# Performance work log

Measured on AMD Instinct MI355X. Metric: run time of the kernel, lower is better.

Reference implementation:

```python
import jax, jax.numpy as jnp
import numpy as np


def quat_to_rot(q):
    # q: [B, 4] = (x, y, z, w); same math as from_quaternion in the source.
    x, y, z, w = q[:, 0], q[:, 1], q[:, 2], q[:, 3]
    tx, ty, tz = 2.0 * x, 2.0 * y, 2.0 * z
    twx, twy, twz = tx * w, ty * w, tz * w
    txx, txy, txz = tx * x, ty * x, tz * x
    tyy, tyz, tzz = ty * y, tz * y, tz * z
    r = jnp.stack([1.0 - (tyy + tzz), txy - twz, txz + twy,
                   txy + twz, 1.0 - (txx + tzz), tyz - twx,
                   txz - twy, tyz + twx, 1.0 - (txx + tyy)], axis=-1)
    return r.reshape(-1, 3, 3)


def matrix_from_params(transfos):
    B, N = transfos.shape
    R = quat_to_rot(transfos[:, :4])
    if N == 10:
        S = jax.vmap(jnp.diag)(transfos[:, -3:])
    else:
        S = jnp.broadcast_to(jnp.eye(3, dtype=transfos.dtype), (B, 3, 3))
    SR = jnp.matmul(S, R)
    if N == 7:
        t = transfos[:, 4:7][..., None]
    else:
        t = jnp.zeros((B, 3, 1), transfos.dtype)
    return jnp.concatenate([SR, t], axis=2)  # [B, 3, 4]


def spatial_transformer_3d(img, transfos, min_ref_grid, max_ref_grid):
    B, H, W, D, C = img.shape  # ref_size_xyz = (W, H, D) per the source
    theta = matrix_from_params(transfos)  # [B, 3, 4]

    xs = jnp.linspace(min_ref_grid[0], max_ref_grid[0], W)
    ys = jnp.linspace(min_ref_grid[1], max_ref_grid[1], H)
    zs = jnp.linspace(min_ref_grid[2], max_ref_grid[2], D)
    mz, my, mx = jnp.meshgrid(zs, ys, xs, indexing='ij')  # (D, H, W), x fastest
    Nel = D * H * W
    grid = jnp.stack([mx.ravel(), my.ravel(), mz.ravel(),
                      jnp.ones(Nel, dtype=img.dtype)], axis=0)  # (4, Nel)
    pts = jnp.einsum('bij,jn->bin', theta, grid)  # (B, 3, Nel)

    Wf, Hf, Df = float(W), float(H), float(D)
    cx = (Wf - 1.0) / (max_ref_grid[0] - min_ref_grid[0])
    cy = (Hf - 1.0) / (max_ref_grid[1] - min_ref_grid[1])
    cz = (Df - 1.0) / (max_ref_grid[2] - min_ref_grid[2])
    ix = cx * pts[:, 0, :] - cx * min_ref_grid[0]
    iy = cy * pts[:, 1, :] - cy * min_ref_grid[1]
    iz = cz * pts[:, 2, :] - cz * min_ref_grid[2]

    # padding_mode in {'zeros','min'}: validity mask for out-of-grid points
    valid = ((ix >= 0.0) & (ix <= Wf - 1.0) &
             (iy >= 0.0) & (iy <= Hf - 1.0) &
             (iz >= 0.0) & (iz <= Df - 1.0)).astype(img.dtype)[..., None]  # (B, Nel, 1)

    ix0 = jnp.clip(jnp.floor(ix), 0.0, Wf - 1.0)
    iy0 = jnp.clip(jnp.floor(iy), 0.0, Hf - 1.0)
    iz0 = jnp.clip(jnp.floor(iz), 0.0, Df - 1.0)

    imf = img.reshape(B, H * W * D, C)
    acc = jnp.zeros((B, Nel, C), img.dtype)
    for ox in (0.0, 1.0):
        for oy in (0.0, 1.0):
            for oz in (0.0, 1.0):
                gx, gy, gz = ix0 + ox, iy0 + oy, iz0 + oz  # corner coords
                w = (jnp.clip(1.0 - jnp.abs(ix - gx), 0.0, 1.0) *
                     jnp.clip(1.0 - jnp.abs(iy - gy), 0.0, 1.0) *
                     jnp.clip(1.0 - jnp.abs(iz - gz), 0.0, 1.0))
                gxi = jnp.clip(gx, 0.0, Wf - 1.0).astype(jnp.int32)
                gyi = jnp.clip(gy, 0.0, Hf - 1.0).astype(jnp.int32)
                gzi = jnp.clip(gz, 0.0, Df - 1.0).astype(jnp.int32)
                lin = (gyi * W + gxi) * D + gzi  # row-major index into [H, W, D]
                v = jnp.take_along_axis(imf, lin[..., None], axis=1)  # (B, Nel, C)
                acc = acc + w[..., None] * v

    # padding_mode == 'min': fill out-of-grid voxels with the per-volume minimum
    fill = jnp.min(img, axis=(1, 2, 3, 4))[:, None, None]  # (B, 1, 1)
    out = valid * acc + (1.0 - valid) * fill
    # grid was flattened in (z, y, x) order with x fastest -> back to (H, W, D)
    out = out.reshape(B, D, H, W, C).transpose(0, 2, 3, 1, 4)
    return out


def setup_inputs() -> dict:
    key = jax.random.key(0)
    k1, k2 = jax.random.split(key)
    img = jax.random.normal(k1, (4, 160, 160, 160, 1), dtype=jnp.float32)
    transfos = jax.random.normal(k2, (4, 7), dtype=jnp.float32)
    return {"img": img, "transfos": transfos}


def reference(img, transfos):
    min_ref_grid = (-1.0, -1.0, -1.0)
    max_ref_grid = (1.0, 1.0, 1.0)
    return spatial_transformer_3d(img, transfos, min_ref_grid, max_ref_grid)
```

## Files before the change

### kernel.cpp

```cpp
#include <hip/hip_runtime.h>

#define HH 160
#define WW 160
#define DD 160
#define BB 4
#define NPB (HH * WW * DD / 4)
#define K1B 256

typedef float vfloat4 __attribute__((ext_vector_type(4)));

__global__ __launch_bounds__(256) void min_cst_kernel(const float4* __restrict__ img4,
                                                      const float* __restrict__ transfos,
                                                      float* __restrict__ partial,
                                                      double* __restrict__ cst) {
    const int b = blockIdx.y;
    const size_t base = (size_t)b * NPB;
    const int t0 = blockIdx.x * 256 + threadIdx.x;
    const int S = K1B * 256;

    float m = 3.4e38f;
    #pragma unroll
    for (int r = 0; r < 4; r++) {
        const int i0 = t0 + 4 * r * S;
        float4 v0 = img4[base + i0];
        float4 v1 = img4[base + i0 + S];
        float4 v2 = img4[base + i0 + 2 * S];
        float4 v3 = make_float4(3.4e38f, 3.4e38f, 3.4e38f, 3.4e38f);
        if (i0 + 3 * S < NPB) v3 = img4[base + i0 + 3 * S];
        m = fminf(m, fminf(fminf(v0.x, v0.y), fminf(v0.z, v0.w)));
        m = fminf(m, fminf(fminf(v1.x, v1.y), fminf(v1.z, v1.w)));
        m = fminf(m, fminf(fminf(v2.x, v2.y), fminf(v2.z, v2.w)));
        m = fminf(m, fminf(fminf(v3.x, v3.y), fminf(v3.z, v3.w)));
    }

    #pragma unroll
    for (int o = 32; o >= 1; o >>= 1) m = fminf(m, __shfl_down(m, o));
    __shared__ float s[4];
    const int lane = threadIdx.x & 63, wid = threadIdx.x >> 6;
    if (lane == 0) s[wid] = m;
    __syncthreads();
    if (threadIdx.x == 0) {
        partial[b * K1B + blockIdx.x] =
            fminf(fminf(s[0], s[1]), fminf(s[2], s[3]));
    }

    if (blockIdx.x == 0 && blockIdx.y == 0 && threadIdx.x < BB) {
        const int bb = threadIdx.x;
        const float* q = transfos + bb * 7;
        double x = q[0], y = q[1], z = q[2], w = q[3];
        double tx = 2.0 * x, ty = 2.0 * y, tz = 2.0 * z;
        double twx = tx * w, twy = ty * w, twz = tz * w;
        double txx = tx * x, txy = ty * x, txz = tz * x;
        double tyy = ty * y, tyz = tz * y, tzz = tz * z;
        double R[3][3] = {
            {1.0 - (tyy + tzz), txy - twz,         txz + twy},
            {txy + twz,         1.0 - (txx + tzz), tyz - twx},
            {txz - twy,         tyz + twx,         1.0 - (txx + tyy)}
        };
        double t[3] = {(double)q[4], (double)q[5], (double)q[6]};
        for (int r = 0; r < 3; r++) {
            cst[bb * 12 + r * 4 + 0] = R[r][0];
            cst[bb * 12 + r * 4 + 1] = R[r][1];
            cst[bb * 12 + r * 4 + 2] = R[r][2];
            cst[bb * 12 + r * 4 + 3] = 79.5 * (t[r] - R[r][0] - R[r][1] - R[r][2] + 1.0);
        }
    }
}

__global__ __launch_bounds__(256) void fin_min_kernel(const float* __restrict__ partial,
                                                      float* __restrict__ fill) {
    const int wid = threadIdx.x >> 6, lane = threadIdx.x & 63;
    const float* p = partial + wid * K1B;
    float m = fminf(fminf(p[lane], p[lane + 64]), fminf(p[lane + 128], p[lane + 192]));
    #pragma unroll
    for (int o = 32; o >= 1; o >>= 1) m = fminf(m, __shfl_down(m, o));
    if (lane == 0) fill[wid] = m;
}

__global__ __launch_bounds__(256) void fill_kernel(const float* __restrict__ fill,
                                                   float* __restrict__ out) {
    const int b = blockIdx.y;
    const float fv = fill[b];
    vfloat4 v; v[0] = fv; v[1] = fv; v[2] = fv; v[3] = fv;
    vfloat4* o = (vfloat4*)(out + (size_t)b * (HH * WW * DD));
    const int stride = gridDim.x * 256;
    for (int i = blockIdx.x * 256 + threadIdx.x; i < NPB; i += stride)
        __builtin_nontemporal_store(v, o + i);
}

__global__ __launch_bounds__(256) void st3d_kernel(const float* __restrict__ img,
                                                   const double* __restrict__ cst,
                                                   const float* __restrict__ fill,
                                                   float* __restrict__ out) {
    const int bzc = blockIdx.z;
    const int b = bzc / 20;
    const int yt = bzc - b * 20;

    const double* c = cst + b * 12;
    const double c2 = c[2], c6 = c[6], c10 = c[10];

    {
        const double X0 = (double)(blockIdx.y * 8), X1 = X0 + 7.0;
        const double Y0 = (double)(yt * 8),         Y1 = Y0 + 7.0;
        const double Z0 = (double)(blockIdx.x * 16), Z1 = Z0 + 15.0;
        double lo, hi, t;

        lo = c[3]; hi = c[3];
        t = c[0]; if (t >= 0.0) { lo += t * X0; hi += t * X1; } else { lo += t * X1; hi += t * X0; }
        t = c[1]; if (t >= 0.0) { lo += t * Y0; hi += t * Y1; } else { lo += t * Y1; hi += t * Y0; }
        t = c2;   if (t >= 0.0) { lo += t * Z0; hi += t * Z1; } else { lo += t * Z1; hi += t * Z0; }
        if (hi < -1e-3 || lo > 159.001) return;

        lo = c[7]; hi = c[7];
        t = c[4]; if (t >= 0.0) { lo += t * X0; hi += t * X1; } else { lo += t * X1; hi += t * X0; }
        t = c[5]; if (t >= 0.0) { lo += t * Y0; hi += t * Y1; } else { lo += t * Y1; hi += t * Y0; }
        t = c6;   if (t >= 0.0) { lo += t * Z0; hi += t * Z1; } else { lo += t * Z1; hi += t * Z0; }
        if (hi < -1e-3 || lo > 159.001) return;

        lo = c[11]; hi = c[11];
        t = c[8]; if (t >= 0.0) { lo += t * X0; hi += t * X1; } else { lo += t * X1; hi += t * X0; }
        t = c[9]; if (t >= 0.0) { lo += t * Y0; hi += t * Y1; } else { lo += t * Y1; hi += t * Y0; }
        t = c10;  if (t >= 0.0) { lo += t * Z0; hi += t * Z1; } else { lo += t * Z1; hi += t * Z0; }
        if (hi < -1e-3 || lo > 159.001) return;
    }

    const int tz = threadIdx.x & 3;
    const int tx = (threadIdx.x >> 2) & 7;
    const int ty = threadIdx.x >> 5;

    const int x  = blockIdx.y * 8 + tx;
    const int y  = yt * 8 + ty;
    const int zq = blockIdx.x * 16 + tz * 4;

    const float fillv = fill[b];

    const double dx = (double)x, dy = (double)y, dz = (double)zq;
    double ixd = fma(c[0], dx, fma(c[1], dy, fma(c2, dz, c[3])));
    double iyd = fma(c[4], dx, fma(c[5], dy, fma(c6, dz, c[7])));
    double izd = fma(c[8], dx, fma(c[9], dy, fma(c10, dz, c[11])));

    bool anyv = false;
    {
        double ax = ixd, ay = iyd, az = izd;
        #pragma unroll
        for (int k = 0; k < 4; k++) {
            anyv = anyv || ((ax >= 0.0) && (ax <= 159.0) && (ay >= 0.0) &&
                            (ay <= 159.0) && (az >= 0.0) && (az <= 159.0));
            ax += c2; ay += c6; az += c10;
        }
    }

    const float* base = img + (size_t)b * (HH * WW * DD);
    vfloat4 r;

    if (__any(anyv)) {
        #pragma unroll
        for (int k = 0; k < 4; k++) {
            const bool valid = (ixd >= 0.0) && (ixd <= 159.0) && (iyd >= 0.0) &&
                               (iyd <= 159.0) && (izd >= 0.0) && (izd <= 159.0);
            double flx = floor(ixd), fly = floor(iyd), flz = floor(izd);
            int x0 = (int)flx, y0 = (int)fly, z0 = (int)flz;
            x0 = min(max(x0, 0), 159);
            y0 = min(max(y0, 0), 159);
            z0 = min(max(z0, 0), 159);
            float fx = (float)(ixd - flx), fy = (float)(iyd - fly), fz = (float)(izd - flz);
            int x1 = min(x0 + 1, 159), y1 = min(y0 + 1, 159), z1 = min(z0 + 1, 159);
            const int o00 = (y0 * WW + x0) * DD;
            const int o01 = (y0 * WW + x1) * DD;
            const int o10 = (y1 * WW + x0) * DD;
            const int o11 = (y1 * WW + x1) * DD;
            float v000 = base[o00 + z0], v001 = base[o00 + z1];
            float v010 = base[o10 + z0], v011 = base[o10 + z1];
            float v100 = base[o01 + z0], v101 = base[o01 + z1];
            float v110 = base[o11 + z0], v111 = base[o11 + z1];
            float wx0 = 1.0f - fx, wx1 = fx;
            float wy0 = 1.0f - fy, wy1 = fy;
            float wz0 = 1.0f - fz, wz1 = fz;
            float acc;
            acc  = ((wx0 * wy0) * wz0) * v000;
            acc += ((wx0 * wy0) * wz1) * v001;
            acc += ((wx0 * wy1) * wz0) * v010;
            acc += ((wx0 * wy1) * wz1) * v011;
            acc += ((wx1 * wy0) * wz0) * v100;
            acc += ((wx1 * wy0) * wz1) * v101;
            acc += ((wx1 * wy1) * wz0) * v110;
            acc += ((wx1 * wy1) * wz1) * v111;
            r[k] = valid ? acc : fillv;
            ixd += c2; iyd += c6; izd += c10;
        }
    } else {
        r[0] = fillv; r[1] = fillv; r[2] = fillv; r[3] = fillv;
    }

    vfloat4* outp = (vfloat4*)(out + (size_t)((b * HH + y) * WW + x) * DD + zq);
    __builtin_nontemporal_store(r, outp);
}

extern "C" void kernel_launch(void* const* d_in, const int* in_sizes, int n_in,
                              void* d_out, int out_size, void* d_ws, size_t ws_size,
                              hipStream_t stream) {
    const float* img = (const float*)d_in[0];
    const float* transfos = (const float*)d_in[1];
    float* out = (float*)d_out;
    float* partial = (float*)d_ws;
    double* cst = (double*)((char*)d_ws + 4096);
    float* fill = (float*)((char*)d_ws + 8192);

    min_cst_kernel<<<dim3(K1B, BB), 256, 0, stream>>>((const float4*)img, transfos,
                                                      partial, cst);
    fin_min_kernel<<<dim3(1), 256, 0, stream>>>(partial, fill);
    fill_kernel<<<dim3(512, BB), 256, 0, stream>>>(fill, out);
    st3d_kernel<<<dim3(DD / 16, WW / 8, (HH / 8) * BB), 256, 0, stream>>>(img, cst,
                                                                          fill, out);
}
```

Measured before the change: 144.3 us.

## Classify tiles, fill only invalid ones, gather over compacted job list

A classification kernel tests each tile against the transformed volume bounds. Tiles that cannot be valid get the fill value written directly. Candidate tiles are appended to a compacted job list through an atomic counter, and a persistent gather kernel processes that list with one wave per two-row slab. This removes the separate full-volume fill pass that the valid tiles later overwrite, and it avoids launching mostly-idle blocks for the gather. In exchange it adds an atomic, an extra workspace requirement, and job-decode overhead, and it falls back to the old path when the workspace is too small.

After: 135.3 us. -6.2%, faster.

```diff
diff --git a/kernel.cpp b/kernel.cpp
--- a/kernel.cpp
+++ b/kernel.cpp
@@ -6,6 +6,12 @@
 #define BB 4
 #define NPB (HH * WW * DD / 4)
 #define K1B 256
+#define NTZ 10
+#define NTX 20
+#define NTY 20
+#define NTILES (BB * NTY * NTX * NTZ)
+#define JCAP (NTILES * 4)
+#define GBLK 2048
 
 typedef float vfloat4 __attribute__((ext_vector_type(4)));
 
@@ -68,13 +74,167 @@
 }
 
 __global__ __launch_bounds__(256) void fin_min_kernel(const float* __restrict__ partial,
-                                                      float* __restrict__ fill) {
+                                                      float* __restrict__ fill,
+                                                      int* __restrict__ counter) {
+    if (threadIdx.x == 0) *counter = 0;
     const int wid = threadIdx.x >> 6, lane = threadIdx.x & 63;
     const float* p = partial + wid * K1B;
     float m = fminf(fminf(p[lane], p[lane + 64]), fminf(p[lane + 128], p[lane + 192]));
     #pragma unroll
     for (int o = 32; o >= 1; o >>= 1) m = fminf(m, __shfl_down(m, o));
     if (lane == 0) fill[wid] = m;
+}
+
+__device__ __forceinline__ bool tile_may_be_valid(const double* c, int xt, int yt, int zt) {
+    const double X0 = (double)(xt * 8), X1 = X0 + 7.0;
+    const double Y0 = (double)(yt * 8), Y1 = Y0 + 7.0;
+    const double Z0 = (double)(zt * 16), Z1 = Z0 + 15.0;
+    double lo, hi, t;
+
+    lo = c[3]; hi = c[3];
+    t = c[0]; if (t >= 0.0) { lo += t * X0; hi += t * X1; } else { lo += t * X1; hi += t * X0; }
+    t = c[1]; if (t >= 0.0) { lo += t * Y0; hi += t * Y1; } else { lo += t * Y1; hi += t * Y0; }
+    t = c[2]; if (t >= 0.0) { lo += t * Z0; hi += t * Z1; } else { lo += t * Z1; hi += t * Z0; }
+    if (hi < -1e-3 || lo > 159.001) return false;
+
+    lo = c[7]; hi = c[7];
+    t = c[4]; if (t >= 0.0) { lo += t * X0; hi += t * X1; } else { lo += t * X1; hi += t * X0; }
+    t = c[5]; if (t >= 0.0) { lo += t * Y0; hi += t * Y1; } else { lo += t * Y1; hi += t * Y0; }
+    t = c[6]; if (t >= 0.0) { lo += t * Z0; hi += t * Z1; } else { lo += t * Z1; hi += t * Z0; }
+    if (hi < -1e-3 || lo > 159.001) return false;
+
+    lo = c[11]; hi = c[11];
+    t = c[8]; if (t >= 0.0) { lo += t * X0; hi += t * X1; } else { lo += t * X1; hi += t * X0; }
+    t = c[9]; if (t >= 0.0) { lo += t * Y0; hi += t * Y1; } else { lo += t * Y1; hi += t * Y0; }
+    t = c[10]; if (t >= 0.0) { lo += t * Z0; hi += t * Z1; } else { lo += t * Z1; hi += t * Z0; }
+    if (hi < -1e-3 || lo > 159.001) return false;
+    return true;
+}
+
+__global__ __launch_bounds__(256) void fill_cls_kernel(const double* __restrict__ cst,
+                                                       const float* __restrict__ fill,
+                                                       float* __restrict__ out,
+                                                       int* __restrict__ counter,
+                                                       int* __restrict__ list) {
+    const int bzc = blockIdx.z;
+    const int b = bzc / NTY;
+    const int yt = bzc - b * NTY;
+    const double* c = cst + b * 12;
+
+    if (tile_may_be_valid(c, blockIdx.y, yt, blockIdx.x)) {
+        if (threadIdx.x == 0) {
+            const int t = ((b * NTY + yt) * NTX + blockIdx.y) * NTZ + blockIdx.x;
+            const int idx = atomicAdd(counter, 4);
+            list[idx + 0] = t * 4 + 0;
+            list[idx + 1] = t * 4 + 1;
+            list[idx + 2] = t * 4 + 2;
+            list[idx + 3] = t * 4 + 3;
+        }
+        return;
+    }
+
+    const float fv = fill[b];
+    vfloat4 v; v[0] = fv; v[1] = fv; v[2] = fv; v[3] = fv;
+    const int tz = threadIdx.x & 3;
+    const int tx = (threadIdx.x >> 2) & 7;
+    const int ty = threadIdx.x >> 5;
+    const int x = blockIdx.y * 8 + tx;
+    const int y = yt * 8 + ty;
+    const int zq = blockIdx.x * 16 + tz * 4;
+    __builtin_nontemporal_store(v, (vfloat4*)(out + (size_t)((b * HH + y) * WW + x) * DD + zq));
+}
+
+__global__ __launch_bounds__(256) void gather_kernel(const float* __restrict__ img,
+                                                     const double* __restrict__ cst,
+                                                     const float* __restrict__ fill,
+                                                     float* __restrict__ out,
+                                                     const int* __restrict__ counter,
+                                                     const int* __restrict__ list) {
+    const int cnt = *counter;
+    const int wid = threadIdx.x >> 6;
+    const int lane = threadIdx.x & 63;
+    const int tz = lane & 3;
+    const int tx = (lane >> 2) & 7;
+    const int tyl = lane >> 5;
+    const int nslots = gridDim.x * 4;
+
+    for (int j = blockIdx.x * 4 + wid; j < cnt; j += nslots) {
+        const int job = list[j];
+        const int t = job >> 2, pair = job & 3;
+        int zt = t % NTZ;
+        int r0i = t / NTZ;
+        int xt = r0i % NTX; r0i /= NTX;
+        int yt = r0i % NTY;
+        const int b = r0i / NTY;
+
+        const int x = xt * 8 + tx;
+        const int y = yt * 8 + pair * 2 + tyl;
+        const int zq = zt * 16 + tz * 4;
+
+        const double* c = cst + b * 12;
+        const double c2 = c[2], c6 = c[6], c10 = c[10];
+        const float fillv = fill[b];
+
+        const double dx = (double)x, dy = (double)y, dz = (double)zq;
+        double ixd = fma(c[0], dx, fma(c[1], dy, fma(c2, dz, c[3])));
+        double iyd = fma(c[4], dx, fma(c[5], dy, fma(c6, dz, c[7])));
+        double izd = fma(c[8], dx, fma(c[9], dy, fma(c10, dz, c[11])));
+
+        bool anyv = false;
+        {
+            double ax = ixd, ay = iyd, az = izd;
+            #pragma unroll
+            for (int k = 0; k < 4; k++) {
+                anyv = anyv || ((ax >= 0.0) && (ax <= 159.0) && (ay >= 0.0) &&
+                                (ay <= 159.0) && (az >= 0.0) && (az <= 159.0));
+                ax += c2; ay += c6; az += c10;
+            }
+        }
+
+        const float* base = img + (size_t)b * (HH * WW * DD);
+        vfloat4 r;
+
+        if (__any(anyv)) {
+            #pragma unroll
+            for (int k = 0; k < 4; k++) {
+                const bool valid = (ixd >= 0.0) && (ixd <= 159.0) && (iyd >= 0.0) &&
+                                   (iyd <= 159.0) && (izd >= 0.0) && (izd <= 159.0);
+                double flx = floor(ixd), fly = floor(iyd), flz = floor(izd);
+                int x0 = (int)flx, y0 = (int)fly, z0 = (int)flz;
+                x0 = min(max(x0, 0), 159);
+                y0 = min(max(y0, 0), 159);
+                z0 = min(max(z0, 0), 159);
+                float fx = (float)(ixd - flx), fy = (float)(iyd - fly), fz = (float)(izd - flz);
+                int x1 = min(x0 + 1, 159), y1 = min(y0 + 1, 159), z1 = min(z0 + 1, 159);
+                const int o00 = (y0 * WW + x0) * DD;
+                const int o01 = (y0 * WW + x1) * DD;
+                const int o10 = (y1 * WW + x0) * DD;
+                const int o11 = (y1 * WW + x1) * DD;
+                float v000 = base[o00 + z0], v001 = base[o00 + z1];
+                float v010 = base[o10 + z0], v011 = base[o10 + z1];
+                float v100 = base[o01 + z0], v101 = base[o01 + z1];
+                float v110 = base[o11 + z0], v111 = base[o11 + z1];
+                float wx0 = 1.0f - fx, wx1 = fx;
+                float wy0 = 1.0f - fy, wy1 = fy;
+                float wz0 = 1.0f - fz, wz1 = fz;
+                float acc;
+                acc  = ((wx0 * wy0) * wz0) * v000;
+                acc += ((wx0 * wy0) * wz1) * v001;
+                acc += ((wx0 * wy1) * wz0) * v010;
+                acc += ((wx0 * wy1) * wz1) * v011;
+                acc += ((wx1 * wy0) * wz0) * v100;
+                acc += ((wx1 * wy0) * wz1) * v101;
+                acc += ((wx1 * wy1) * wz0) * v110;
+                acc += ((wx1 * wy1) * wz1) * v111;
+                r[k] = valid ? acc : fillv;
+                ixd += c2; iyd += c6; izd += c10;
+            }
+        } else {
+            r[0] = fillv; r[1] = fillv; r[2] = fillv; r[3] = fillv;
+        }
+
+        __builtin_nontemporal_store(r, (vfloat4*)(out + (size_t)((b * HH + y) * WW + x) * DD + zq));
+    }
 }
 
 __global__ __launch_bounds__(256) void fill_kernel(const float* __restrict__ fill,
@@ -88,50 +248,23 @@
         __builtin_nontemporal_store(v, o + i);
 }
 
-__global__ __launch_bounds__(256) void st3d_kernel(const float* __restrict__ img,
-                                                   const double* __restrict__ cst,
-                                                   const float* __restrict__ fill,
-                                                   float* __restrict__ out) {
+__global__ __launch_bounds__(256) void st3d_tile_kernel(const float* __restrict__ img,
+                                                        const double* __restrict__ cst,
+                                                        const float* __restrict__ fill,
+                                                        float* __restrict__ out) {
     const int bzc = blockIdx.z;
-    const int b = bzc / 20;
-    const int yt = bzc - b * 20;
-
+    const int b = bzc / NTY;
+    const int yt = bzc - b * NTY;
     const double* c = cst + b * 12;
+    if (!tile_may_be_valid(c, blockIdx.y, yt, blockIdx.x)) return;
+
     const double c2 = c[2], c6 = c[6], c10 = c[10];
-
-    {
-        const double X0 = (double)(blockIdx.y * 8), X1 = X0 + 7.0;
-        const double Y0 = (double)(yt * 8),         Y1 = Y0 + 7.0;
-        const double Z0 = (double)(blockIdx.x * 16), Z1 = Z0 + 15.0;
-        double lo, hi, t;
-
-        lo = c[3]; hi = c[3];
-        t = c[0]; if (t >= 0.0) { lo += t * X0; hi += t * X1; } else { lo += t * X1; hi += t * X0; }
-        t = c[1]; if (t >= 0.0) { lo += t * Y0; hi += t * Y1; } else { lo += t * Y1; hi += t * Y0; }
-        t = c2;   if (t >= 0.0) { lo += t * Z0; hi += t * Z1; } else { lo += t * Z1; hi += t * Z0; }
-        if (hi < -1e-3 || lo > 159.001) return;
-
-        lo = c[7]; hi = c[7];
-        t = c[4]; if (t >= 0.0) { lo += t * X0; hi += t * X1; } else { lo += t * X1; hi += t * X0; }
-        t = c[5]; if (t >= 0.0) { lo += t * Y0; hi += t * Y1; } else { lo += t * Y1; hi += t * Y0; }
-        t = c6;   if (t >= 0.0) { lo += t * Z0; hi += t * Z1; } else { lo += t * Z1; hi += t * Z0; }
-        if (hi < -1e-3 || lo > 159.001) return;
-
-        lo = c[11]; hi = c[11];
-        t = c[8]; if (t >= 0.0) { lo += t * X0; hi += t * X1; } else { lo += t * X1; hi += t * X0; }
-        t = c[9]; if (t >= 0.0) { lo += t * Y0; hi += t * Y1; } else { lo += t * Y1; hi += t * Y0; }
-        t = c10;  if (t >= 0.0) { lo += t * Z0; hi += t * Z1; } else { lo += t * Z1; hi += t * Z0; }
-        if (hi < -1e-3 || lo > 159.001) return;
-    }
-
     const int tz = threadIdx.x & 3;
     const int tx = (threadIdx.x >> 2) & 7;
     const int ty = threadIdx.x >> 5;
-
-    const int x  = blockIdx.y * 8 + tx;
-    const int y  = yt * 8 + ty;
+    const int x = blockIdx.y * 8 + tx;
+    const int y = yt * 8 + ty;
     const int zq = blockIdx.x * 16 + tz * 4;
-
     const float fillv = fill[b];
 
     const double dx = (double)x, dy = (double)y, dz = (double)zq;
@@ -152,7 +285,6 @@
 
     const float* base = img + (size_t)b * (HH * WW * DD);
     vfloat4 r;
-
     if (__any(anyv)) {
         #pragma unroll
         for (int k = 0; k < 4; k++) {
@@ -191,9 +323,7 @@
     } else {
         r[0] = fillv; r[1] = fillv; r[2] = fillv; r[3] = fillv;
     }
-
-    vfloat4* outp = (vfloat4*)(out + (size_t)((b * HH + y) * WW + x) * DD + zq);
-    __builtin_nontemporal_store(r, outp);
+    __builtin_nontemporal_store(r, (vfloat4*)(out + (size_t)((b * HH + y) * WW + x) * DD + zq));
 }
 
 extern "C" void kernel_launch(void* const* d_in, const int* in_sizes, int n_in,
@@ -205,11 +335,19 @@
     float* partial = (float*)d_ws;
     double* cst = (double*)((char*)d_ws + 4096);
     float* fill = (float*)((char*)d_ws + 8192);
+    int* counter = (int*)((char*)d_ws + 8448);
+    int* list = (int*)((char*)d_ws + 8704);
 
     min_cst_kernel<<<dim3(K1B, BB), 256, 0, stream>>>((const float4*)img, transfos,
                                                       partial, cst);
-    fin_min_kernel<<<dim3(1), 256, 0, stream>>>(partial, fill);
-    fill_kernel<<<dim3(512, BB), 256, 0, stream>>>(fill, out);
-    st3d_kernel<<<dim3(DD / 16, WW / 8, (HH / 8) * BB), 256, 0, stream>>>(img, cst,
-                                                                          fill, out);
-}
+    fin_min_kernel<<<dim3(1), 256, 0, stream>>>(partial, fill, counter);
+
+    if (ws_size >= (size_t)(8704 + JCAP * 4)) {
+        fill_cls_kernel<<<dim3(NTZ, NTX, NTY * BB), 256, 0, stream>>>(cst, fill, out,
+                                                                      counter, list);
+        gather_kernel<<<dim3(GBLK), 256, 0, stream>>>(img, cst, fill, out, counter, list);
+    } else {
+        fill_kernel<<<dim3(512, BB), 256, 0, stream>>>(fill, out);
+        st3d_tile_kernel<<<dim3(NTZ, NTX, NTY * BB), 256, 0, stream>>>(img, cst, fill, out);
+    }
+}
```

## Fuse min-reduction, fill and gather into one cooperative persistent kernel

Applied to the files above, without the earlier changes.

Replaces the four-launch pipeline (min reduction, final min, fill, gather) with a single cooperative kernel. It computes the per-batch minimum through an atomicMin on an order-preserving encoded float, uses a grid-wide sync, then loops over tiles and writes either the fill value or gathered samples, so the output is written once instead of twice. The gather also reads each z-pair as one 8-byte load instead of two scalar loads. Risks include the grid-sync cost, the residency requirement of 1024 blocks (the old multi-kernel path remains as a fallback if the cooperative launch fails), and an added memset.

New measurement: 238.9 us. 1.66x slower.

```diff
diff --git a/kernel.cpp b/kernel.cpp
--- a/kernel.cpp
+++ b/kernel.cpp
@@ -1,4 +1,5 @@
 #include <hip/hip_runtime.h>
+#include <hip/hip_cooperative_groups.h>
 
 #define HH 160
 #define WW 160
@@ -6,8 +7,217 @@
 #define BB 4
 #define NPB (HH * WW * DD / 4)
 #define K1B 256
+#define NTZ 10
+#define NTX 20
+#define NTY 20
+#define NTILES (BB * NTY * NTX * NTZ)
+#define GRID 1024
 
 typedef float vfloat4 __attribute__((ext_vector_type(4)));
+
+__device__ __forceinline__ unsigned enc_f32(float f) {
+    unsigned u = __float_as_uint(f);
+    return u ^ ((u & 0x80000000u) ? 0xFFFFFFFFu : 0x80000000u);
+}
+__device__ __forceinline__ float dec_f32(unsigned e) {
+    return __uint_as_float(e ^ ((e & 0x80000000u) ? 0x80000000u : 0xFFFFFFFFu));
+}
+
+__device__ __forceinline__ bool tile_may_be_valid(const double* c, int xt, int yt, int zt) {
+    const double X0 = (double)(xt * 8), X1 = X0 + 7.0;
+    const double Y0 = (double)(yt * 8), Y1 = Y0 + 7.0;
+    const double Z0 = (double)(zt * 16), Z1 = Z0 + 15.0;
+    double lo, hi, t;
+
+    lo = c[3]; hi = c[3];
+    t = c[0]; if (t >= 0.0) { lo += t * X0; hi += t * X1; } else { lo += t * X1; hi += t * X0; }
+    t = c[1]; if (t >= 0.0) { lo += t * Y0; hi += t * Y1; } else { lo += t * Y1; hi += t * Y0; }
+    t = c[2]; if (t >= 0.0) { lo += t * Z0; hi += t * Z1; } else { lo += t * Z1; hi += t * Z0; }
+    if (hi < -1e-3 || lo > 159.001) return false;
+
+    lo = c[7]; hi = c[7];
+    t = c[4]; if (t >= 0.0) { lo += t * X0; hi += t * X1; } else { lo += t * X1; hi += t * X0; }
+    t = c[5]; if (t >= 0.0) { lo += t * Y0; hi += t * Y1; } else { lo += t * Y1; hi += t * Y0; }
+    t = c[6]; if (t >= 0.0) { lo += t * Z0; hi += t * Z1; } else { lo += t * Z1; hi += t * Z0; }
+    if (hi < -1e-3 || lo > 159.001) return false;
+
+    lo = c[11]; hi = c[11];
+    t = c[8]; if (t >= 0.0) { lo += t * X0; hi += t * X1; } else { lo += t * X1; hi += t * X0; }
+    t = c[9]; if (t >= 0.0) { lo += t * Y0; hi += t * Y1; } else { lo += t * Y1; hi += t * Y0; }
+    t = c[10]; if (t >= 0.0) { lo += t * Z0; hi += t * Z1; } else { lo += t * Z1; hi += t * Z0; }
+    if (hi < -1e-3 || lo > 159.001) return false;
+    return true;
+}
+
+__device__ __forceinline__ void gather_tile(const float* __restrict__ img,
+                                            const double* __restrict__ c,
+                                            float fillv, int b, int xt, int yt, int zt,
+                                            int tid, float* __restrict__ out)
+{
+    const int tz = tid & 3;
+    const int tx = (tid >> 2) & 7;
+    const int ty = tid >> 5;
+    const int x = xt * 8 + tx;
+    const int y = yt * 8 + ty;
+    const int zq = zt * 16 + tz * 4;
+
+    const double c2 = c[2], c6 = c[6], c10 = c[10];
+    const double dx = (double)x, dy = (double)y, dz = (double)zq;
+    double ixd = fma(c[0], dx, fma(c[1], dy, fma(c2, dz, c[3])));
+    double iyd = fma(c[4], dx, fma(c[5], dy, fma(c6, dz, c[7])));
+    double izd = fma(c[8], dx, fma(c[9], dy, fma(c10, dz, c[11])));
+
+    bool anyv = false;
+    {
+        double ax = ixd, ay = iyd, az = izd;
+        #pragma unroll
+        for (int k = 0; k < 4; k++) {
+            anyv = anyv || ((ax >= 0.0) && (ax <= 159.0) && (ay >= 0.0) &&
+                            (ay <= 159.0) && (az >= 0.0) && (az <= 159.0));
+            ax += c2; ay += c6; az += c10;
+        }
+    }
+
+    const float* base = img + (size_t)b * (HH * WW * DD);
+    vfloat4 r;
+
+    if (__any(anyv)) {
+        #pragma unroll
+        for (int k = 0; k < 4; k++) {
+            const bool valid = (ixd >= 0.0) && (ixd <= 159.0) && (iyd >= 0.0) &&
+                               (iyd <= 159.0) && (izd >= 0.0) && (izd <= 159.0);
+            double flx = floor(ixd), fly = floor(iyd), flz = floor(izd);
+            int x0 = (int)flx, y0 = (int)fly, z0 = (int)flz;
+            x0 = min(max(x0, 0), 159);
+            y0 = min(max(y0, 0), 159);
+            z0 = min(max(z0, 0), 159);
+            float fx = (float)(ixd - flx), fy = (float)(iyd - fly), fz = (float)(izd - flz);
+            int x1 = min(x0 + 1, 159), y1 = min(y0 + 1, 159);
+            const int zb = min(z0, 158);
+            const bool ztop = (z0 == 159);
+            const float* p00 = base + (y0 * WW + x0) * DD + zb;
+            const float* p10 = base + (y1 * WW + x0) * DD + zb;
+            const float* p01 = base + (y0 * WW + x1) * DD + zb;
+            const float* p11 = base + (y1 * WW + x1) * DD + zb;
+            float2 q00, q10, q01, q11;
+            __builtin_memcpy(&q00, p00, 8);
+            __builtin_memcpy(&q10, p10, 8);
+            __builtin_memcpy(&q01, p01, 8);
+            __builtin_memcpy(&q11, p11, 8);
+            float v000 = ztop ? q00.y : q00.x, v001 = q00.y;
+            float v010 = ztop ? q10.y : q10.x, v011 = q10.y;
+            float v100 = ztop ? q01.y : q01.x, v101 = q01.y;
+            float v110 = ztop ? q11.y : q11.x, v111 = q11.y;
+            float wx0 = 1.0f - fx, wx1 = fx;
+            float wy0 = 1.0f - fy, wy1 = fy;
+            float wz0 = 1.0f - fz, wz1 = fz;
+            float acc;
+            acc  = ((wx0 * wy0) * wz0) * v000;
+            acc += ((wx0 * wy0) * wz1) * v001;
+            acc += ((wx0 * wy1) * wz0) * v010;
+            acc += ((wx0 * wy1) * wz1) * v011;
+            acc += ((wx1 * wy0) * wz0) * v100;
+            acc += ((wx1 * wy0) * wz1) * v101;
+            acc += ((wx1 * wy1) * wz0) * v110;
+            acc += ((wx1 * wy1) * wz1) * v111;
+            r[k] = valid ? acc : fillv;
+            ixd += c2; iyd += c6; izd += c10;
+        }
+    } else {
+        r[0] = fillv; r[1] = fillv; r[2] = fillv; r[3] = fillv;
+    }
+
+    __builtin_nontemporal_store(r, (vfloat4*)(out + (size_t)((b * HH + y) * WW + x) * DD + zq));
+}
+
+__global__ __launch_bounds__(256, 4) void fused_kernel(const float* __restrict__ img,
+                                                       const float* __restrict__ transfos,
+                                                       unsigned* __restrict__ fillEnc,
+                                                       double* __restrict__ cst,
+                                                       float* __restrict__ out) {
+    const int bid = blockIdx.x;
+    const int tid = threadIdx.x;
+
+    {
+        const float4* img4 = (const float4*)img;
+        const int b = bid >> 8;
+        const int bx = bid & 255;
+        const size_t base = (size_t)b * NPB;
+        const int t0 = bx * 256 + tid;
+        const int S = K1B * 256;
+
+        float m = 3.4e38f;
+        #pragma unroll
+        for (int r = 0; r < 4; r++) {
+            const int i0 = t0 + 4 * r * S;
+            float4 v0 = img4[base + i0];
+            float4 v1 = img4[base + i0 + S];
+            float4 v2 = img4[base + i0 + 2 * S];
+            float4 v3 = make_float4(3.4e38f, 3.4e38f, 3.4e38f, 3.4e38f);
+            if (i0 + 3 * S < NPB) v3 = img4[base + i0 + 3 * S];
+            m = fminf(m, fminf(fminf(v0.x, v0.y), fminf(v0.z, v0.w)));
+            m = fminf(m, fminf(fminf(v1.x, v1.y), fminf(v1.z, v1.w)));
+            m = fminf(m, fminf(fminf(v2.x, v2.y), fminf(v2.z, v2.w)));
+            m = fminf(m, fminf(fminf(v3.x, v3.y), fminf(v3.z, v3.w)));
+        }
+        #pragma unroll
+        for (int o = 32; o >= 1; o >>= 1) m = fminf(m, __shfl_down(m, o));
+        __shared__ float s[4];
+        if ((tid & 63) == 0) s[tid >> 6] = m;
+        __syncthreads();
+        if (tid == 0) {
+            float bm = fminf(fminf(s[0], s[1]), fminf(s[2], s[3]));
+            atomicMin(&fillEnc[b], enc_f32(bm));
+        }
+
+        if (bid == 0 && tid < BB) {
+            const int bb = tid;
+            const float* q = transfos + bb * 7;
+            double x = q[0], y = q[1], z = q[2], w = q[3];
+            double tx = 2.0 * x, ty = 2.0 * y, tz = 2.0 * z;
+            double twx = tx * w, twy = ty * w, twz = tz * w;
+            double txx = tx * x, txy = ty * x, txz = tz * x;
+            double tyy = ty * y, tyz = tz * y, tzz = tz * z;
+            double R[3][3] = {
+                {1.0 - (tyy + tzz), txy - twz,         txz + twy},
+                {txy + twz,         1.0 - (txx + tzz), tyz - twx},
+                {txz - twy,         tyz + twx,         1.0 - (txx + tyy)}
+            };
+            double tr[3] = {(double)q[4], (double)q[5], (double)q[6]};
+            for (int r = 0; r < 3; r++) {
+                cst[bb * 12 + r * 4 + 0] = R[r][0];
+                cst[bb * 12 + r * 4 + 1] = R[r][1];
+                cst[bb * 12 + r * 4 + 2] = R[r][2];
+                cst[bb * 12 + r * 4 + 3] = 79.5 * (tr[r] - R[r][0] - R[r][1] - R[r][2] + 1.0);
+            }
+        }
+    }
+
+    cooperative_groups::this_grid().sync();
+
+    for (int t = bid; t < NTILES; t += GRID) {
+        int zt = t % NTZ;
+        int rr = t / NTZ;
+        int xt = rr % NTX; rr /= NTX;
+        int yt = rr % NTY;
+        const int b = rr / NTY;
+        const double* c = cst + b * 12;
+        const float fillv = dec_f32(fillEnc[b]);
+
+        if (tile_may_be_valid(c, xt, yt, zt)) {
+            gather_tile(img, c, fillv, b, xt, yt, zt, tid, out);
+        } else {
+            vfloat4 v; v[0] = fillv; v[1] = fillv; v[2] = fillv; v[3] = fillv;
+            const int tz = tid & 3;
+            const int tx = (tid >> 2) & 7;
+            const int ty = tid >> 5;
+            const int x = xt * 8 + tx;
+            const int y = yt * 8 + ty;
+            const int zq = zt * 16 + tz * 4;
+            __builtin_nontemporal_store(v, (vfloat4*)(out + (size_t)((b * HH + y) * WW + x) * DD + zq));
+        }
+    }
+}
 
 __global__ __launch_bounds__(256) void min_cst_kernel(const float4* __restrict__ img4,
                                                       const float* __restrict__ transfos,
@@ -32,17 +242,13 @@
         m = fminf(m, fminf(fminf(v2.x, v2.y), fminf(v2.z, v2.w)));
         m = fminf(m, fminf(fminf(v3.x, v3.y), fminf(v3.z, v3.w)));
     }
-
     #pragma unroll
     for (int o = 32; o >= 1; o >>= 1) m = fminf(m, __shfl_down(m, o));
     __shared__ float s[4];
-    const int lane = threadIdx.x & 63, wid = threadIdx.x >> 6;
-    if (lane == 0) s[wid] = m;
+    if ((threadIdx.x & 63) == 0) s[threadIdx.x >> 6] = m;
     __syncthreads();
-    if (threadIdx.x == 0) {
-        partial[b * K1B + blockIdx.x] =
-            fminf(fminf(s[0], s[1]), fminf(s[2], s[3]));
-    }
+    if (threadIdx.x == 0)
+        partial[b * K1B + blockIdx.x] = fminf(fminf(s[0], s[1]), fminf(s[2], s[3]));
 
     if (blockIdx.x == 0 && blockIdx.y == 0 && threadIdx.x < BB) {
         const int bb = threadIdx.x;
@@ -88,112 +294,16 @@
         __builtin_nontemporal_store(v, o + i);
 }
 
-__global__ __launch_bounds__(256) void st3d_kernel(const float* __restrict__ img,
-                                                   const double* __restrict__ cst,
-                                                   const float* __restrict__ fill,
-                                                   float* __restrict__ out) {
+__global__ __launch_bounds__(256) void st3d_tile_kernel(const float* __restrict__ img,
+                                                        const double* __restrict__ cst,
+                                                        const float* __restrict__ fill,
+                                                        float* __restrict__ out) {
     const int bzc = blockIdx.z;
-    const int b = bzc / 20;
-    const int yt = bzc - b * 20;
-
+    const int b = bzc / NTY;
+    const int yt = bzc - b * NTY;
     const double* c = cst + b * 12;
-    const double c2 = c[2], c6 = c[6], c10 = c[10];
-
-    {
-        const double X0 = (double)(blockIdx.y * 8), X1 = X0 + 7.0;
-        const double Y0 = (double)(yt * 8),         Y1 = Y0 + 7.0;
-        const double Z0 = (double)(blockIdx.x * 16), Z1 = Z0 + 15.0;
-        double lo, hi, t;
-
-        lo = c[3]; hi = c[3];
-        t = c[0]; if (t >= 0.0) { lo += t * X0; hi += t * X1; } else { lo += t * X1; hi += t * X0; }
-        t = c[1]; if (t >= 0.0) { lo += t * Y0; hi += t * Y1; } else { lo += t * Y1; hi += t * Y0; }
-        t = c2;   if (t >= 0.0) { lo += t * Z0; hi += t * Z1; } else { lo += t * Z1; hi += t * Z0; }
-        if (hi < -1e-3 || lo > 159.001) return;
-
-        lo = c[7]; hi = c[7];
-        t = c[4]; if (t >= 0.0) { lo += t * X0; hi += t * X1; } else { lo += t * X1; hi += t * X0; }
-        t = c[5]; if (t >= 0.0) { lo += t * Y0; hi += t * Y1; } else { lo += t * Y1; hi += t * Y0; }
-        t = c6;   if (t >= 0.0) { lo += t * Z0; hi += t * Z1; } else { lo += t * Z1; hi += t * Z0; }
-        if (hi < -1e-3 || lo > 159.001) return;
-
-        lo = c[11]; hi = c[11];
-        t = c[8]; if (t >= 0.0) { lo += t * X0; hi += t * X1; } else { lo += t * X1; hi += t * X0; }
-        t = c[9]; if (t >= 0.0) { lo += t * Y0; hi += t * Y1; } else { lo += t * Y1; hi += t * Y0; }
-        t = c10;  if (t >= 0.0) { lo += t * Z0; hi += t * Z1; } else { lo += t * Z1; hi += t * Z0; }
-        if (hi < -1e-3 || lo > 159.001) return;
-    }
-
-    const int tz = threadIdx.x & 3;
-    const int tx = (threadIdx.x >> 2) & 7;
-    const int ty = threadIdx.x >> 5;
-
-    const int x  = blockIdx.y * 8 + tx;
-    const int y  = yt * 8 + ty;
-    const int zq = blockIdx.x * 16 + tz * 4;
-
-    const float fillv = fill[b];
-
-    const double dx = (double)x, dy = (double)y, dz = (double)zq;
-    double ixd = fma(c[0], dx, fma(c[1], dy, fma(c2, dz, c[3])));
-    double iyd = fma(c[4], dx, fma(c[5], dy, fma(c6, dz, c[7])));
-    double izd = fma(c[8], dx, fma(c[9], dy, fma(c10, dz, c[11])));
-
-    bool anyv = false;
-    {
-        double ax = ixd, ay = iyd, az = izd;
-        #pragma unroll
-        for (int k = 0; k < 4; k++) {
-            anyv = anyv || ((ax >= 0.0) && (ax <= 159.0) && (ay >= 0.0) &&
-                            (ay <= 159.0) && (az >= 0.0) && (az <= 159.0));
-            ax += c2; ay += c6; az += c10;
-        }
-    }
-
-    const float* base = img + (size_t)b * (HH * WW * DD);
-    vfloat4 r;
-
-    if (__any(anyv)) {
-        #pragma unroll
-        for (int k = 0; k < 4; k++) {
-            const bool valid = (ixd >= 0.0) && (ixd <= 159.0) && (iyd >= 0.0) &&
-                               (iyd <= 159.0) && (izd >= 0.0) && (izd <= 159.0);
-            double flx = floor(ixd), fly = floor(iyd), flz = floor(izd);
-            int x0 = (int)flx, y0 = (int)fly, z0 = (int)flz;
-            x0 = min(max(x0, 0), 159);
-            y0 = min(max(y0, 0), 159);
-            z0 = min(max(z0, 0), 159);
-            float fx = (float)(ixd - flx), fy = (float)(iyd - fly), fz = (float)(izd - flz);
-            int x1 = min(x0 + 1, 159), y1 = min(y0 + 1, 159), z1 = min(z0 + 1, 159);
-            const int o00 = (y0 * WW + x0) * DD;
-            const int o01 = (y0 * WW + x1) * DD;
-            const int o10 = (y1 * WW + x0) * DD;
-            const int o11 = (y1 * WW + x1) * DD;
-            float v000 = base[o00 + z0], v001 = base[o00 + z1];
-            float v010 = base[o10 + z0], v011 = base[o10 + z1];
-            float v100 = base[o01 + z0], v101 = base[o01 + z1];
-            float v110 = base[o11 + z0], v111 = base[o11 + z1];
-            float wx0 = 1.0f - fx, wx1 = fx;
-            float wy0 = 1.0f - fy, wy1 = fy;
-            float wz0 = 1.0f - fz, wz1 = fz;
-            float acc;
-            acc  = ((wx0 * wy0) * wz0) * v000;
-            acc += ((wx0 * wy0) * wz1) * v001;
-            acc += ((wx0 * wy1) * wz0) * v010;
-            acc += ((wx0 * wy1) * wz1) * v011;
-            acc += ((wx1 * wy0) * wz0) * v100;
-            acc += ((wx1 * wy0) * wz1) * v101;
-            acc += ((wx1 * wy1) * wz0) * v110;
-            acc += ((wx1 * wy1) * wz1) * v111;
-            r[k] = valid ? acc : fillv;
-            ixd += c2; iyd += c6; izd += c10;
-        }
-    } else {
-        r[0] = fillv; r[1] = fillv; r[2] = fillv; r[3] = fillv;
-    }
-
-    vfloat4* outp = (vfloat4*)(out + (size_t)((b * HH + y) * WW + x) * DD + zq);
-    __builtin_nontemporal_store(r, outp);
+    if (!tile_may_be_valid(c, blockIdx.y, yt, blockIdx.x)) return;
+    gather_tile(img, c, fill[b], b, blockIdx.y, yt, blockIdx.x, threadIdx.x, out);
 }
 
 extern "C" void kernel_launch(void* const* d_in, const int* in_sizes, int n_in,
@@ -202,14 +312,25 @@
     const float* img = (const float*)d_in[0];
     const float* transfos = (const float*)d_in[1];
     float* out = (float*)d_out;
-    float* partial = (float*)d_ws;
-    double* cst = (double*)((char*)d_ws + 4096);
-    float* fill = (float*)((char*)d_ws + 8192);
-
-    min_cst_kernel<<<dim3(K1B, BB), 256, 0, stream>>>((const float4*)img, transfos,
-                                                      partial, cst);
-    fin_min_kernel<<<dim3(1), 256, 0, stream>>>(partial, fill);
-    fill_kernel<<<dim3(512, BB), 256, 0, stream>>>(fill, out);
-    st3d_kernel<<<dim3(DD / 16, WW / 8, (HH / 8) * BB), 256, 0, stream>>>(img, cst,
-                                                                          fill, out);
-}
+
+    unsigned* fillEnc = (unsigned*)d_ws;
+    double* cstC = (double*)((char*)d_ws + 256);
+    float* partial = (float*)((char*)d_ws + 4096);
+    double* cstF = (double*)((char*)d_ws + 9216);
+    float* fillF = (float*)((char*)d_ws + 9728);
+
+    hipMemsetAsync(d_ws, 0xFF, 16, stream);
+
+    void* args[] = { (void*)&img, (void*)&transfos, (void*)&fillEnc,
+                     (void*)&cstC, (void*)&out };
+    hipError_t err = hipLaunchCooperativeKernel((const void*)fused_kernel,
+                                                dim3(GRID), dim3(256), args, 0, stream);
+    if (err != hipSuccess) {
+        min_cst_kernel<<<dim3(K1B, BB), 256, 0, stream>>>((const float4*)img, transfos,
+                                                          partial, cstF);
+        fin_min_kernel<<<dim3(1), 256, 0, stream>>>(partial, fillF);
+        fill_kernel<<<dim3(512, BB), 256, 0, stream>>>(fillF, out);
+        st3d_tile_kernel<<<dim3(NTZ, NTX, NTY * BB), 256, 0, stream>>>(img, cstF,
+                                                                       fillF, out);
+    }
+}
```

## Fuse fill pass into gather kernel and load z-pairs as float2

Applied to the files above, without the earlier changes.

Removes the separate fill kernel, which wrote the whole output volume before the gather kernel overwrote the valid tiles. Tiles that cannot be valid now write the fill value directly inside the gather kernel, so each output element is stored exactly once. The eight scalar corner loads are replaced by four 8-byte loads of adjacent z values, with a clamp and select at the top z edge. This saves one full output write pass and some load instructions, at the cost of possibly unaligned 8-byte loads.

Result: faster. 129.2 us (median of 2 runs) (-10.4%).

```diff
diff --git a/kernel.cpp b/kernel.cpp
--- a/kernel.cpp
+++ b/kernel.cpp
@@ -6,6 +6,9 @@
 #define BB 4
 #define NPB (HH * WW * DD / 4)
 #define K1B 256
+#define NTZ 10
+#define NTX 20
+#define NTY 20
 
 typedef float vfloat4 __attribute__((ext_vector_type(4)));
 
@@ -36,13 +39,10 @@
     #pragma unroll
     for (int o = 32; o >= 1; o >>= 1) m = fminf(m, __shfl_down(m, o));
     __shared__ float s[4];
-    const int lane = threadIdx.x & 63, wid = threadIdx.x >> 6;
-    if (lane == 0) s[wid] = m;
+    if ((threadIdx.x & 63) == 0) s[threadIdx.x >> 6] = m;
     __syncthreads();
-    if (threadIdx.x == 0) {
-        partial[b * K1B + blockIdx.x] =
-            fminf(fminf(s[0], s[1]), fminf(s[2], s[3]));
-    }
+    if (threadIdx.x == 0)
+        partial[b * K1B + blockIdx.x] = fminf(fminf(s[0], s[1]), fminf(s[2], s[3]));
 
     if (blockIdx.x == 0 && blockIdx.y == 0 && threadIdx.x < BB) {
         const int bb = threadIdx.x;
@@ -77,63 +77,45 @@
     if (lane == 0) fill[wid] = m;
 }
 
-__global__ __launch_bounds__(256) void fill_kernel(const float* __restrict__ fill,
-                                                   float* __restrict__ out) {
-    const int b = blockIdx.y;
-    const float fv = fill[b];
-    vfloat4 v; v[0] = fv; v[1] = fv; v[2] = fv; v[3] = fv;
-    vfloat4* o = (vfloat4*)(out + (size_t)b * (HH * WW * DD));
-    const int stride = gridDim.x * 256;
-    for (int i = blockIdx.x * 256 + threadIdx.x; i < NPB; i += stride)
-        __builtin_nontemporal_store(v, o + i);
-}
-
-__global__ __launch_bounds__(256) void st3d_kernel(const float* __restrict__ img,
-                                                   const double* __restrict__ cst,
-                                                   const float* __restrict__ fill,
-                                                   float* __restrict__ out) {
-    const int bzc = blockIdx.z;
-    const int b = bzc / 20;
-    const int yt = bzc - b * 20;
-
-    const double* c = cst + b * 12;
+__device__ __forceinline__ bool tile_may_be_valid(const double* c, int xt, int yt, int zt) {
+    const double X0 = (double)(xt * 8), X1 = X0 + 7.0;
+    const double Y0 = (double)(yt * 8), Y1 = Y0 + 7.0;
+    const double Z0 = (double)(zt * 16), Z1 = Z0 + 15.0;
+    double lo, hi, t;
+
+    lo = c[3]; hi = c[3];
+    t = c[0]; if (t >= 0.0) { lo += t * X0; hi += t * X1; } else { lo += t * X1; hi += t * X0; }
+    t = c[1]; if (t >= 0.0) { lo += t * Y0; hi += t * Y1; } else { lo += t * Y1; hi += t * Y0; }
+    t = c[2]; if (t >= 0.0) { lo += t * Z0; hi += t * Z1; } else { lo += t * Z1; hi += t * Z0; }
+    if (hi < -1e-3 || lo > 159.001) return false;
+
+    lo = c[7]; hi = c[7];
+    t = c[4]; if (t >= 0.0) { lo += t * X0; hi += t * X1; } else { lo += t * X1; hi += t * X0; }
+    t = c[5]; if (t >= 0.0) { lo += t * Y0; hi += t * Y1; } else { lo += t * Y1; hi += t * Y0; }
+    t = c[6]; if (t >= 0.0) { lo += t * Z0; hi += t * Z1; } else { lo += t * Z1; hi += t * Z0; }
+    if (hi < -1e-3 || lo > 159.001) return false;
+
+    lo = c[11]; hi = c[11];
+    t = c[8]; if (t >= 0.0) { lo += t * X0; hi += t * X1; } else { lo += t * X1; hi += t * X0; }
+    t = c[9]; if (t >= 0.0) { lo += t * Y0; hi += t * Y1; } else { lo += t * Y1; hi += t * Y0; }
+    t = c[10]; if (t >= 0.0) { lo += t * Z0; hi += t * Z1; } else { lo += t * Z1; hi += t * Z0; }
+    if (hi < -1e-3 || lo > 159.001) return false;
+    return true;
+}
+
+__device__ __forceinline__ void gather_tile(const float* __restrict__ img,
+                                            const double* __restrict__ c,
+                                            float fillv, int b, int xt, int yt, int zt,
+                                            int tid, float* __restrict__ out)
+{
+    const int tz = tid & 3;
+    const int tx = (tid >> 2) & 7;
+    const int ty = tid >> 5;
+    const int x = xt * 8 + tx;
+    const int y = yt * 8 + ty;
+    const int zq = zt * 16 + tz * 4;
+
     const double c2 = c[2], c6 = c[6], c10 = c[10];
-
-    {
-        const double X0 = (double)(blockIdx.y * 8), X1 = X0 + 7.0;
-        const double Y0 = (double)(yt * 8),         Y1 = Y0 + 7.0;
-        const double Z0 = (double)(blockIdx.x * 16), Z1 = Z0 + 15.0;
-        double lo, hi, t;
-
-        lo = c[3]; hi = c[3];
-        t = c[0]; if (t >= 0.0) { lo += t * X0; hi += t * X1; } else { lo += t * X1; hi += t * X0; }
-        t = c[1]; if (t >= 0.0) { lo += t * Y0; hi += t * Y1; } else { lo += t * Y1; hi += t * Y0; }
-        t = c2;   if (t >= 0.0) { lo += t * Z0; hi += t * Z1; } else { lo += t * Z1; hi += t * Z0; }
-        if (hi < -1e-3 || lo > 159.001) return;
-
-        lo = c[7]; hi = c[7];
-        t = c[4]; if (t >= 0.0) { lo += t * X0; hi += t * X1; } else { lo += t * X1; hi += t * X0; }
-        t = c[5]; if (t >= 0.0) { lo += t * Y0; hi += t * Y1; } else { lo += t * Y1; hi += t * Y0; }
-        t = c6;   if (t >= 0.0) { lo += t * Z0; hi += t * Z1; } else { lo += t * Z1; hi += t * Z0; }
-        if (hi < -1e-3 || lo > 159.001) return;
-
-        lo = c[11]; hi = c[11];
-        t = c[8]; if (t >= 0.0) { lo += t * X0; hi += t * X1; } else { lo += t * X1; hi += t * X0; }
-        t = c[9]; if (t >= 0.0) { lo += t * Y0; hi += t * Y1; } else { lo += t * Y1; hi += t * Y0; }
-        t = c10;  if (t >= 0.0) { lo += t * Z0; hi += t * Z1; } else { lo += t * Z1; hi += t * Z0; }
-        if (hi < -1e-3 || lo > 159.001) return;
-    }
-
-    const int tz = threadIdx.x & 3;
-    const int tx = (threadIdx.x >> 2) & 7;
-    const int ty = threadIdx.x >> 5;
-
-    const int x  = blockIdx.y * 8 + tx;
-    const int y  = yt * 8 + ty;
-    const int zq = blockIdx.x * 16 + tz * 4;
-
-    const float fillv = fill[b];
-
     const double dx = (double)x, dy = (double)y, dz = (double)zq;
     double ixd = fma(c[0], dx, fma(c[1], dy, fma(c2, dz, c[3])));
     double iyd = fma(c[4], dx, fma(c[5], dy, fma(c6, dz, c[7])));
@@ -164,15 +146,22 @@
             y0 = min(max(y0, 0), 159);
             z0 = min(max(z0, 0), 159);
             float fx = (float)(ixd - flx), fy = (float)(iyd - fly), fz = (float)(izd - flz);
-            int x1 = min(x0 + 1, 159), y1 = min(y0 + 1, 159), z1 = min(z0 + 1, 159);
-            const int o00 = (y0 * WW + x0) * DD;
-            const int o01 = (y0 * WW + x1) * DD;
-            const int o10 = (y1 * WW + x0) * DD;
-            const int o11 = (y1 * WW + x1) * DD;
-            float v000 = base[o00 + z0], v001 = base[o00 + z1];
-            float v010 = base[o10 + z0], v011 = base[o10 + z1];
-            float v100 = base[o01 + z0], v101 = base[o01 + z1];
-            float v110 = base[o11 + z0], v111 = base[o11 + z1];
+            int x1 = min(x0 + 1, 159), y1 = min(y0 + 1, 159);
+            const int zb = min(z0, 158);
+            const bool ztop = (z0 == 159);
+            const float* p00 = base + (y0 * WW + x0) * DD + zb;
+            const float* p10 = base + (y1 * WW + x0) * DD + zb;
+            const float* p01 = base + (y0 * WW + x1) * DD + zb;
+            const float* p11 = base + (y1 * WW + x1) * DD + zb;
+            float2 q00, q10, q01, q11;
+            __builtin_memcpy(&q00, p00, 8);
+            __builtin_memcpy(&q10, p10, 8);
+            __builtin_memcpy(&q01, p01, 8);
+            __builtin_memcpy(&q11, p11, 8);
+            float v000 = ztop ? q00.y : q00.x, v001 = q00.y;
+            float v010 = ztop ? q10.y : q10.x, v011 = q10.y;
+            float v100 = ztop ? q01.y : q01.x, v101 = q01.y;
+            float v110 = ztop ? q11.y : q11.x, v111 = q11.y;
             float wx0 = 1.0f - fx, wx1 = fx;
             float wy0 = 1.0f - fy, wy1 = fy;
             float wz0 = 1.0f - fz, wz1 = fz;
@@ -192,8 +181,33 @@
         r[0] = fillv; r[1] = fillv; r[2] = fillv; r[3] = fillv;
     }
 
-    vfloat4* outp = (vfloat4*)(out + (size_t)((b * HH + y) * WW + x) * DD + zq);
-    __builtin_nontemporal_store(r, outp);
+    __builtin_nontemporal_store(r, (vfloat4*)(out + (size_t)((b * HH + y) * WW + x) * DD + zq));
+}
+
+__global__ __launch_bounds__(256) void st3d_kernel(const float* __restrict__ img,
+                                                   const double* __restrict__ cst,
+                                                   const float* __restrict__ fill,
+                                                   float* __restrict__ out) {
+    const int bzc = blockIdx.z;
+    const int b = bzc / NTY;
+    const int yt = bzc - b * NTY;
+    const int xt = blockIdx.y;
+    const int zt = blockIdx.x;
+    const double* c = cst + b * 12;
+    const float fillv = fill[b];
+
+    if (tile_may_be_valid(c, xt, yt, zt)) {
+        gather_tile(img, c, fillv, b, xt, yt, zt, threadIdx.x, out);
+    } else {
+        vfloat4 v; v[0] = fillv; v[1] = fillv; v[2] = fillv; v[3] = fillv;
+        const int tz = threadIdx.x & 3;
+        const int tx = (threadIdx.x >> 2) & 7;
+        const int ty = threadIdx.x >> 5;
+        const int x = xt * 8 + tx;
+        const int y = yt * 8 + ty;
+        const int zq = zt * 16 + tz * 4;
+        __builtin_nontemporal_store(v, (vfloat4*)(out + (size_t)((b * HH + y) * WW + x) * DD + zq));
+    }
 }
 
 extern "C" void kernel_launch(void* const* d_in, const int* in_sizes, int n_in,
@@ -209,7 +223,5 @@
     min_cst_kernel<<<dim3(K1B, BB), 256, 0, stream>>>((const float4*)img, transfos,
                                                       partial, cst);
     fin_min_kernel<<<dim3(1), 256, 0, stream>>>(partial, fill);
-    fill_kernel<<<dim3(512, BB), 256, 0, stream>>>(fill, out);
-    st3d_kernel<<<dim3(DD / 16, WW / 8, (HH / 8) * BB), 256, 0, stream>>>(img, cst,
-                                                                          fill, out);
-}
+    st3d_kernel<<<dim3(NTZ, NTX, NTY * BB), 256, 0, stream>>>(img, cst, fill, out);
+}
```
